# Kernel tuning notes

Hardware: AMD Instinct MI355X
Metric: run time of the kernel (lower is better)

The kernel has to match this reference:

```python
import jax, jax.numpy as jnp
import numpy as np

N = 50000          # nodes
E = 625000         # edges
H = 128            # hidden_dim
L = 4              # num_layers
G = 2000           # number of graphs in batch
NODE_F = 9
EDGE_F = 4
LN_EPS = 1e-5


def setup_inputs() -> dict:
    key = jax.random.key(0)
    ks = jax.random.split(key, 14)
    s = 0.05
    return {
        "x": jax.random.normal(ks[0], (N, NODE_F), jnp.float32),
        "edge_index": jax.random.randint(ks[1], (2, E), 0, N, dtype=jnp.int32),
        "edge_attr": jax.random.normal(ks[2], (E, EDGE_F), jnp.float32),
        "batch": jnp.sort(jax.random.randint(ks[3], (N,), 0, G, dtype=jnp.int32)),
        # node / edge encoders
        "Wn": jax.random.normal(ks[4], (NODE_F, H), jnp.float32) * s,
        "bn": jnp.zeros((H,), jnp.float32),
        "We": jax.random.normal(ks[5], (EDGE_F, H), jnp.float32) * s,
        "be": jnp.zeros((H,), jnp.float32),
        # per-layer GINE MLP params (stacked over layers)
        "W1": jax.random.normal(ks[6], (L, H, 2 * H), jnp.float32) * s,
        "b1": jnp.zeros((L, 2 * H), jnp.float32),
        "W2": jax.random.normal(ks[7], (L, 2 * H, H), jnp.float32) * s,
        "b2": jnp.zeros((L, H), jnp.float32),
        # per-layer LayerNorm params
        "gamma": jnp.ones((L, H), jnp.float32),
        "beta": jnp.zeros((L, H), jnp.float32),
    }


def reference(x, edge_index, edge_attr, batch, Wn, bn, We, be, W1, b1, W2, b2, gamma, beta):
    h = x @ Wn + bn                       # [N, H]
    ea = edge_attr @ We + be              # [E, H]
    src, dst = edge_index[0], edge_index[1]
    for l in range(L):
        res = h
        # GINEConv (eps=0): out = mlp(x + sum_j relu(x_j + e_ij))
        msg = jax.nn.relu(h[src] + ea)                              # [E, H] gather+add+relu
        agg = jax.ops.segment_sum(msg, dst, num_segments=N)        # scatter-sum -> [N, H]
        z = h + agg
        z = jax.nn.relu(z @ W1[l] + b1[l]) @ W2[l] + b2[l]          # 2-layer MLP
        mu = jnp.mean(z, axis=-1, keepdims=True)
        var = jnp.mean((z - mu) ** 2, axis=-1, keepdims=True)
        z = (z - mu) * jax.lax.rsqrt(var + LN_EPS) * gamma[l] + beta[l]
        h = jax.nn.relu(z) + res                                    # relu + residual
    # global_add_pool
    return jax.ops.segment_sum(h, batch, num_segments=G)            # [G, H]
```

## Files before the change

### kernel.cpp

```cpp
#include <hip/hip_runtime.h>

typedef unsigned short ushort_t;
typedef __attribute__((ext_vector_type(8))) __bf16 bf16x8;
typedef __attribute__((ext_vector_type(4))) float f32x4;

#define HD 128
#define NL 4
#define SCAN_C 2048

__device__ __forceinline__ ushort_t f2bf(float f){
  unsigned u = __builtin_bit_cast(unsigned, f);
  unsigned r = (u + 0x7FFFu + ((u >> 16) & 1u)) >> 16;
  return (ushort_t)r;
}

__device__ __forceinline__ float bf2f(ushort_t u){
  unsigned v = ((unsigned)u) << 16;
  return __builtin_bit_cast(float, v);
}

__device__ __forceinline__ f32x4 mfma16(bf16x8 a, bf16x8 b, f32x4 c){
  return __builtin_amdgcn_mfma_f32_16x16x32_bf16(a, b, c, 0, 0, 0);
}

__global__ void hist_kernel(const int* __restrict__ dst, int* __restrict__ deg, int E){
  int e = blockIdx.x * 256 + threadIdx.x;
  if (e < E) atomicAdd(&deg[dst[e]], 1);
}

__global__ void ghist_kernel(const int* __restrict__ batch, int* __restrict__ gdeg, int N){
  int n = blockIdx.x * 256 + threadIdx.x;
  if (n < N) atomicAdd(&gdeg[batch[n]], 1);
}

__global__ void scan_part(const int* __restrict__ in, int* __restrict__ bsum, int n){
  int b = blockIdx.x, tid = threadIdx.x;
  int base = b * SCAN_C + tid * 8;
  int s = 0;
  if (base + 8 <= n){
    int4 a = *(const int4*)(in + base);
    int4 c = *(const int4*)(in + base + 4);
    s = a.x + a.y + a.z + a.w + c.x + c.y + c.z + c.w;
  } else {
    #pragma unroll
    for (int k = 0; k < 8; ++k) if (base + k < n) s += in[base + k];
  }
  #pragma unroll
  for (int o = 1; o < 64; o <<= 1) s += __shfl_xor(s, o, 64);
  __shared__ int ws[4];
  int lane = tid & 63, wid = tid >> 6;
  if (lane == 0) ws[wid] = s;
  __syncthreads();
  if (tid == 0) bsum[b] = ws[0] + ws[1] + ws[2] + ws[3];
}

__global__ void scan_top(const int* __restrict__ bsum, int* __restrict__ bofs,
                         int* __restrict__ outn, int B){
  int tid = threadIdx.x;
  int v = (tid < B) ? bsum[tid] : 0;
  int lane = tid & 63, wid = tid >> 6;
  int inc = v;
  #pragma unroll
  for (int o = 1; o < 64; o <<= 1){
    int t = __shfl_up(inc, o, 64);
    if (lane >= o) inc += t;
  }
  __shared__ int ws[4];
  if (lane == 63) ws[wid] = inc;
  __syncthreads();
  int wprev = 0;
  for (int i = 0; i < wid; ++i) wprev += ws[i];
  if (tid < B) bofs[tid] = inc - v + wprev;
  if (tid == 0) *outn = ws[0] + ws[1] + ws[2] + ws[3];
}

__global__ void scan_final(const int* __restrict__ in, const int* __restrict__ bofs,
                           int* __restrict__ out, int* __restrict__ cur, int n){
  int b = blockIdx.x, tid = threadIdx.x;
  int base = b * SCAN_C + tid * 8;
  int v[8];
  if (base + 8 <= n){
    *(int4*)(v)     = *(const int4*)(in + base);
    *(int4*)(v + 4) = *(const int4*)(in + base + 4);
  } else {
    #pragma unroll
    for (int k = 0; k < 8; ++k) v[k] = (base + k < n) ? in[base + k] : 0;
  }
  int tsum = 0;
  #pragma unroll
  for (int k = 0; k < 8; ++k) tsum += v[k];
  int lane = tid & 63, wid = tid >> 6;
  int inc = tsum;
  #pragma unroll
  for (int o = 1; o < 64; o <<= 1){
    int t = __shfl_up(inc, o, 64);
    if (lane >= o) inc += t;
  }
  __shared__ int ws[4];
  if (lane == 63) ws[wid] = inc;
  __syncthreads();
  int run = bofs[b] + inc - tsum;
  for (int i = 0; i < wid; ++i) run += ws[i];
  #pragma unroll
  for (int k = 0; k < 8; ++k){
    int i = base + k;
    if (i < n){
      out[i] = run;
      if (cur) cur[i] = run;
      run += v[k];
    }
  }
}

__global__ void scatter_kernel(const int* __restrict__ dst, int* __restrict__ cursor,
                               int* __restrict__ perm, int E){
  int e = blockIdx.x * 256 + threadIdx.x;
  if (e < E){
    int d = dst[e];
    int p = atomicAdd(&cursor[d], 1);
    perm[p] = e;
  }
}

__global__ void permute_kernel(const int* __restrict__ perm, const int* __restrict__ src,
                               const float4* __restrict__ ea, int* __restrict__ srcs_s,
                               float4* __restrict__ ea4p, int E){
  int p = blockIdx.x * 256 + threadIdx.x;
  if (p < E){
    int e = perm[p];
    srcs_s[p] = src[e];
    ea4p[p] = ea[e];
  }
}

__global__ void wconv_kernel(const float* __restrict__ W1, const float* __restrict__ W2,
                             ushort_t* __restrict__ W1t, ushort_t* __restrict__ W2t){
  int i = blockIdx.x * 256 + threadIdx.x;
  if (i < NL * 32768){
    int l = i >> 15, r = i & 32767;
    int n = r >> 7, k = r & 127;
    W1t[i] = f2bf(W1[l * 32768 + k * 256 + n]);
  } else {
    int i2 = i - NL * 32768;
    int l = i2 >> 15, r = i2 & 32767;
    int n = r >> 8, k = r & 255;
    W2t[i2] = f2bf(W2[l * 32768 + k * 128 + n]);
  }
}

__global__ void encoder_kernel(const float* __restrict__ x, const float* __restrict__ Wn,
                               const float* __restrict__ bn, float* __restrict__ h,
                               ushort_t* __restrict__ hb, int N){
  int n = blockIdx.x, j = threadIdx.x;
  float acc = bn[j];
  #pragma unroll
  for (int k = 0; k < 9; ++k) acc = fmaf(x[n * 9 + k], Wn[k * HD + j], acc);
  h[(size_t)n * HD + j] = acc;
  hb[(size_t)n * HD + j] = f2bf(acc);
}

__global__ void agg_kernel(const float* __restrict__ h, const ushort_t* __restrict__ hb,
                           const int* __restrict__ off, const int* __restrict__ srcs,
                           const float4* __restrict__ ea4, const float* __restrict__ We,
                           const float* __restrict__ be, ushort_t* __restrict__ z, int N){
  int n = blockIdx.x, j = threadIdx.x;
  float w0 = We[j], w1 = We[HD + j], w2 = We[2 * HD + j], w3 = We[3 * HD + j];
  float bj = be[j];
  int s = off[n], e = off[n + 1];
  float acc = h[(size_t)n * HD + j];
  int i = s;
  for (; i + 8 <= e; i += 8){
    int s0 = srcs[i],     s1 = srcs[i + 1], s2 = srcs[i + 2], s3 = srcs[i + 3];
    int s4 = srcs[i + 4], s5 = srcs[i + 5], s6 = srcs[i + 6], s7 = srcs[i + 7];
    ushort_t g0 = hb[(size_t)s0 * HD + j];
    ushort_t g1 = hb[(size_t)s1 * HD + j];
    ushort_t g2 = hb[(size_t)s2 * HD + j];
    ushort_t g3 = hb[(size_t)s3 * HD + j];
    ushort_t g4 = hb[(size_t)s4 * HD + j];
    ushort_t g5 = hb[(size_t)s5 * HD + j];
    ushort_t g6 = hb[(size_t)s6 * HD + j];
    ushort_t g7 = hb[(size_t)s7 * HD + j];
    {
      float4 a0 = ea4[i], a1 = ea4[i + 1], a2 = ea4[i + 2], a3 = ea4[i + 3];
      float e0 = fmaf(a0.x, w0, fmaf(a0.y, w1, fmaf(a0.z, w2, fmaf(a0.w, w3, bj))));
      float e1 = fmaf(a1.x, w0, fmaf(a1.y, w1, fmaf(a1.z, w2, fmaf(a1.w, w3, bj))));
      float e2 = fmaf(a2.x, w0, fmaf(a2.y, w1, fmaf(a2.z, w2, fmaf(a2.w, w3, bj))));
      float e3 = fmaf(a3.x, w0, fmaf(a3.y, w1, fmaf(a3.z, w2, fmaf(a3.w, w3, bj))));
      acc += fmaxf(bf2f(g0) + e0, 0.f);
      acc += fmaxf(bf2f(g1) + e1, 0.f);
      acc += fmaxf(bf2f(g2) + e2, 0.f);
      acc += fmaxf(bf2f(g3) + e3, 0.f);
    }
    {
      float4 a4 = ea4[i + 4], a5 = ea4[i + 5], a6 = ea4[i + 6], a7 = ea4[i + 7];
      float e4 = fmaf(a4.x, w0, fmaf(a4.y, w1, fmaf(a4.z, w2, fmaf(a4.w, w3, bj))));
      float e5 = fmaf(a5.x, w0, fmaf(a5.y, w1, fmaf(a5.z, w2, fmaf(a5.w, w3, bj))));
      float e6 = fmaf(a6.x, w0, fmaf(a6.y, w1, fmaf(a6.z, w2, fmaf(a6.w, w3, bj))));
      float e7 = fmaf(a7.x, w0, fmaf(a7.y, w1, fmaf(a7.z, w2, fmaf(a7.w, w3, bj))));
      acc += fmaxf(bf2f(g4) + e4, 0.f);
      acc += fmaxf(bf2f(g5) + e5, 0.f);
      acc += fmaxf(bf2f(g6) + e6, 0.f);
      acc += fmaxf(bf2f(g7) + e7, 0.f);
    }
  }
  for (; i + 4 <= e; i += 4){
    int s0 = srcs[i], s1 = srcs[i + 1], s2 = srcs[i + 2], s3 = srcs[i + 3];
    float4 a0 = ea4[i], a1 = ea4[i + 1], a2 = ea4[i + 2], a3 = ea4[i + 3];
    float h0 = bf2f(hb[(size_t)s0 * HD + j]);
    float h1 = bf2f(hb[(size_t)s1 * HD + j]);
    float h2 = bf2f(hb[(size_t)s2 * HD + j]);
    float h3 = bf2f(hb[(size_t)s3 * HD + j]);
    float e0 = fmaf(a0.x, w0, fmaf(a0.y, w1, fmaf(a0.z, w2, fmaf(a0.w, w3, bj))));
    float e1 = fmaf(a1.x, w0, fmaf(a1.y, w1, fmaf(a1.z, w2, fmaf(a1.w, w3, bj))));
    float e2 = fmaf(a2.x, w0, fmaf(a2.y, w1, fmaf(a2.z, w2, fmaf(a2.w, w3, bj))));
    float e3 = fmaf(a3.x, w0, fmaf(a3.y, w1, fmaf(a3.z, w2, fmaf(a3.w, w3, bj))));
    acc += fmaxf(h0 + e0, 0.f);
    acc += fmaxf(h1 + e1, 0.f);
    acc += fmaxf(h2 + e2, 0.f);
    acc += fmaxf(h3 + e3, 0.f);
  }
  for (; i < e; ++i){
    int sc = srcs[i];
    float4 a = ea4[i];
    float eav = fmaf(a.x, w0, fmaf(a.y, w1, fmaf(a.z, w2, fmaf(a.w, w3, bj))));
    acc += fmaxf(bf2f(hb[(size_t)sc * HD + j]) + eav, 0.f);
  }
  z[(size_t)n * HD + j] = f2bf(acc);
}

__global__ __launch_bounds__(512, 4) void mlp_fused_kernel(
    const ushort_t* __restrict__ zin, const ushort_t* __restrict__ W1t,
    const float* __restrict__ b1, const ushort_t* __restrict__ W2t,
    const float* __restrict__ b2, const float* __restrict__ gamma,
    const float* __restrict__ beta, float* __restrict__ h,
    ushort_t* __restrict__ hb, int N){
  extern __shared__ char lds[];
  int tid = threadIdx.x;
  int r0 = blockIdx.x * 128;
  #pragma unroll
  for (int i = 0; i < 4; ++i){
    int g = i * 512 + tid;
    int row = g >> 4, kg = g & 15;
    int lb = row * 256 + ((kg * 16) ^ ((row & 7) << 4));
    int ar = min(r0 + row, N - 1);
    *(bf16x8*)(lds + lb) = *(const bf16x8*)(zin + (size_t)ar * 128 + kg * 8);
  }
  int w = tid >> 6, l = tid & 63;
  int lr = l & 15, lk = l >> 4;
  int wk = w >> 1, wn = w & 1;
  bf16x8 aN[4];
  #pragma unroll
  for (int fm = 0; fm < 4; ++fm)
    aN[fm] = *(const bf16x8*)((const char*)W1t +
              (size_t)(wk * 64 + fm * 16 + lr) * 256 + lk * 16);
  __syncthreads();
  {
    f32x4 acc1[4][4] = {};
    #pragma unroll
    for (int ks = 0; ks < 4; ++ks){
      int kb = ks * 64 + lk * 16;
      bf16x8 aC[4];
      #pragma unroll
      for (int fm = 0; fm < 4; ++fm) aC[fm] = aN[fm];
      if (ks < 3){
        int kbn = (ks + 1) * 64 + lk * 16;
        #pragma unroll
        for (int fm = 0; fm < 4; ++fm)
          aN[fm] = *(const bf16x8*)((const char*)W1t +
                    (size_t)(wk * 64 + fm * 16 + lr) * 256 + kbn);
      }
      bf16x8 b[4];
      #pragma unroll
      for (int fn = 0; fn < 4; ++fn){
        int node = wn * 64 + fn * 16 + lr;
        b[fn] = *(const bf16x8*)(lds + node * 256 + (kb ^ ((node & 7) << 4)));
      }
      #pragma unroll
      for (int fm = 0; fm < 4; ++fm)
        #pragma unroll
        for (int fn = 0; fn < 4; ++fn)
          acc1[fm][fn] = mfma16(aC[fm], b[fn], acc1[fm][fn]);
    }
    __syncthreads();
    #pragma unroll
    for (int fm = 0; fm < 4; ++fm){
      f32x4 bv = *(const f32x4*)(b1 + wk * 64 + fm * 16 + lk * 4);
      int k2b = (wk * 64 + fm * 16 + lk * 4) * 2;
      #pragma unroll
      for (int fn = 0; fn < 4; ++fn){
        int node = wn * 64 + fn * 16 + lr;
        ushort4 tv;
        tv.x = f2bf(fmaxf(acc1[fm][fn][0] + bv[0], 0.f));
        tv.y = f2bf(fmaxf(acc1[fm][fn][1] + bv[1], 0.f));
        tv.z = f2bf(fmaxf(acc1[fm][fn][2] + bv[2], 0.f));
        tv.w = f2bf(fmaxf(acc1[fm][fn][3] + bv[3], 0.f));
        *(ushort4*)(lds + node * 512 + (k2b ^ ((node & 7) << 4))) = tv;
      }
    }
  }
  int wd = w >> 1, wn2 = w & 1;
  bf16x8 a2N[2];
  #pragma unroll
  for (int fm = 0; fm < 2; ++fm)
    a2N[fm] = *(const bf16x8*)((const char*)W2t +
               (size_t)(wd * 32 + fm * 16 + lr) * 512 + lk * 16);
  __syncthreads();
  f32x4 acc2[2][4] = {};
  #pragma unroll
  for (int ks = 0; ks < 8; ++ks){
    int kb = ks * 64 + lk * 16;
    bf16x8 a2C[2];
    #pragma unroll
    for (int fm = 0; fm < 2; ++fm) a2C[fm] = a2N[fm];
    if (ks < 7){
      int kbn = (ks + 1) * 64 + lk * 16;
      #pragma unroll
      for (int fm = 0; fm < 2; ++fm)
        a2N[fm] = *(const bf16x8*)((const char*)W2t +
                   (size_t)(wd * 32 + fm * 16 + lr) * 512 + kbn);
    }
    bf16x8 bt2[4];
    #pragma unroll
    for (int fn = 0; fn < 4; ++fn){
      int node = wn2 * 64 + fn * 16 + lr;
      bt2[fn] = *(const bf16x8*)(lds + node * 512 + (kb ^ ((node & 7) << 4)));
    }
    #pragma unroll
    for (int fm = 0; fm < 2; ++fm)
      #pragma unroll
      for (int fn = 0; fn < 4; ++fn)
        acc2[fm][fn] = mfma16(a2C[fm], bt2[fn], acc2[fm][fn]);
  }
  __syncthreads();
  float* stat_s = (float*)lds;
  float* stat_q = (float*)(lds + 2048);
  f32x4 b2v[2], gv[2], btv[2];
  #pragma unroll
  for (int fm = 0; fm < 2; ++fm){
    int db = wd * 32 + fm * 16 + lk * 4;
    b2v[fm] = *(const f32x4*)(b2 + db);
    gv[fm]  = *(const f32x4*)(gamma + db);
    btv[fm] = *(const f32x4*)(beta + db);
  }
  #pragma unroll
  for (int fn = 0; fn < 4; ++fn){
    float ss = 0.f, qq = 0.f;
    #pragma unroll
    for (int fm = 0; fm < 2; ++fm)
      #pragma unroll
      for (int r = 0; r < 4; ++r){
        float v = acc2[fm][fn][r] + b2v[fm][r];
        acc2[fm][fn][r] = v;
        ss += v; qq += v * v;
      }
    ss += __shfl_xor(ss, 16, 64); ss += __shfl_xor(ss, 32, 64);
    qq += __shfl_xor(qq, 16, 64); qq += __shfl_xor(qq, 32, 64);
    if (l < 16){
      int node = wn2 * 64 + fn * 16 + lr;
      stat_s[node * 4 + wd] = ss;
      stat_q[node * 4 + wd] = qq;
    }
  }
  __syncthreads();
  #pragma unroll
  for (int fn = 0; fn < 4; ++fn){
    int node = wn2 * 64 + fn * 16 + lr;
    int gn = r0 + node;
    float ss = stat_s[node * 4 + 0] + stat_s[node * 4 + 1] +
               stat_s[node * 4 + 2] + stat_s[node * 4 + 3];
    float qq = stat_q[node * 4 + 0] + stat_q[node * 4 + 1] +
               stat_q[node * 4 + 2] + stat_q[node * 4 + 3];
    float mean = ss * (1.f / 128.f);
    float rs = rsqrtf(qq * (1.f / 128.f) - mean * mean + 1e-5f);
    if (gn < N){
      #pragma unroll
      for (int fm = 0; fm < 2; ++fm){
        int db = wd * 32 + fm * 16 + lk * 4;
        f32x4 hold = *(const f32x4*)(h + (size_t)gn * HD + db);
        f32x4 ov;
        #pragma unroll
        for (int r = 0; r < 4; ++r)
          ov[r] = fmaxf((acc2[fm][fn][r] - mean) * rs * gv[fm][r] + btv[fm][r], 0.f) + hold[r];
        *(f32x4*)(h + (size_t)gn * HD + db) = ov;
        ushort4 hv;
        hv.x = f2bf(ov[0]); hv.y = f2bf(ov[1]); hv.z = f2bf(ov[2]); hv.w = f2bf(ov[3]);
        *(ushort4*)(hb + (size_t)gn * HD + db) = hv;
      }
    }
  }
}

__global__ void pool_kernel(const float* __restrict__ h, const int* __restrict__ goff,
                            float* __restrict__ outp, int G){
  int g = blockIdx.x, j = threadIdx.x;
  int s = goff[g], e = goff[g + 1];
  float acc = 0.f;
  for (int i = s; i < e; ++i) acc += h[(size_t)i * HD + j];
  outp[(size_t)g * HD + j] = acc;
}

extern "C" void kernel_launch(void* const* d_in, const int* in_sizes, int n_in,
                              void* d_out, int out_size, void* d_ws, size_t ws_size,
                              hipStream_t stream){
  const float* x     = (const float*)d_in[0];
  const int*   ei    = (const int*)  d_in[1];
  const float* eattr = (const float*)d_in[2];
  const int*   batch = (const int*)  d_in[3];
  const float* Wn    = (const float*)d_in[4];
  const float* bn    = (const float*)d_in[5];
  const float* We    = (const float*)d_in[6];
  const float* be    = (const float*)d_in[7];
  const float* W1    = (const float*)d_in[8];
  const float* b1    = (const float*)d_in[9];
  const float* W2    = (const float*)d_in[10];
  const float* b2    = (const float*)d_in[11];
  const float* gamma = (const float*)d_in[12];
  const float* beta  = (const float*)d_in[13];
  float* outp = (float*)d_out;

  int N = in_sizes[3];
  int E = in_sizes[2] / 4;
  int G = out_size / HD;

  char* base = (char*)d_ws;
  size_t o = 0;
  auto alloc = [&](size_t bytes)->char*{
    char* r = base + o; o = (o + bytes + 255) & ~(size_t)255; return r;
  };
  float*    h    = (float*)   alloc((size_t)N * HD * 4);
  ushort_t* hb   = (ushort_t*)alloc((size_t)N * HD * 2);
  ushort_t* z    = (ushort_t*)alloc((size_t)N * HD * 2);
  ushort_t* W1t  = (ushort_t*)alloc((size_t)NL * 2 * HD * HD * 2);
  ushort_t* W2t  = (ushort_t*)alloc((size_t)NL * 2 * HD * HD * 2);
  int* deg    = (int*)alloc((size_t)N * 4);
  int* gdeg   = (int*)alloc((size_t)G * 4);
  int* off    = (int*)alloc((size_t)(N + 1) * 4);
  int* goff   = (int*)alloc((size_t)(G + 1) * 4);
  int* cursor = (int*)alloc((size_t)N * 4);
  int* bsumN  = (int*)alloc(512 * 4);
  int* bofsN  = (int*)alloc(512 * 4);
  int* bsumG  = (int*)alloc(512 * 4);
  int* bofsG  = (int*)alloc(512 * 4);
  int* perm   = (int*)alloc((size_t)E * 4);
  int* srcs_s = (int*)alloc((size_t)E * 4);
  float4* ea4p= (float4*)alloc((size_t)E * 16);
  (void)ws_size; (void)n_in;

  const int* src = ei;
  const int* dst = ei + E;

  hipMemsetAsync(deg, 0, (size_t)N * 4, stream);
  hipMemsetAsync(gdeg, 0, (size_t)G * 4, stream);

  hist_kernel<<<(E + 255) / 256, 256, 0, stream>>>(dst, deg, E);
  ghist_kernel<<<(N + 255) / 256, 256, 0, stream>>>(batch, gdeg, N);

  int BN = (N + SCAN_C - 1) / SCAN_C;
  int BG = (G + SCAN_C - 1) / SCAN_C;
  scan_part<<<BN, 256, 0, stream>>>(deg, bsumN, N);
  scan_top<<<1, 256, 0, stream>>>(bsumN, bofsN, off + N, BN);
  scan_final<<<BN, 256, 0, stream>>>(deg, bofsN, off, cursor, N);
  scan_part<<<BG, 256, 0, stream>>>(gdeg, bsumG, G);
  scan_top<<<1, 256, 0, stream>>>(bsumG, bofsG, goff + G, BG);
  scan_final<<<BG, 256, 0, stream>>>(gdeg, bofsG, goff, (int*)nullptr, G);

  scatter_kernel<<<(E + 255) / 256, 256, 0, stream>>>(dst, cursor, perm, E);
  permute_kernel<<<(E + 255) / 256, 256, 0, stream>>>(perm, src, (const float4*)eattr,
                                                      srcs_s, ea4p, E);
  wconv_kernel<<<(2 * NL * 32768) / 256, 256, 0, stream>>>(W1, W2, W1t, W2t);
  encoder_kernel<<<N, HD, 0, stream>>>(x, Wn, bn, h, hb, N);

  int mblocks = (N + 127) / 128;
  for (int l = 0; l < NL; ++l){
    agg_kernel<<<N, HD, 0, stream>>>(h, hb, off, srcs_s, ea4p, We, be, z, N);
    mlp_fused_kernel<<<mblocks, 512, 65536, stream>>>(
        z, W1t + (size_t)l * 2 * HD * HD, b1 + l * 2 * HD,
        W2t + (size_t)l * 2 * HD * HD, b2 + l * HD,
        gamma + l * HD, beta + l * HD, h, hb, N);
  }
  pool_kernel<<<G, HD, 0, stream>>>(h, goff, outp, G);
}
```

Before: 421.8 us.

## Use wave-per-node aggregation with paired bf16 loads, derive graph offsets from sorted batch

The aggregation kernel now assigns one 64-lane wave per node instead of a 128-thread block, with each lane handling two adjacent feature channels through 32-bit loads. This halves the number of gather instructions, makes per-edge index and edge-attr loads shared across fewer threads, and packs four nodes per block. The self term now reads the bf16 copy of h instead of the fp32 one, which adds rounding error. Graph offsets for pooling are computed directly from boundaries in the sorted batch array, replacing the histogram plus three scan kernels.

```diff
diff --git a/kernel.cpp b/kernel.cpp
--- a/kernel.cpp
+++ b/kernel.cpp
@@ -28,9 +28,15 @@
   if (e < E) atomicAdd(&deg[dst[e]], 1);
 }
 
-__global__ void ghist_kernel(const int* __restrict__ batch, int* __restrict__ gdeg, int N){
+__global__ void gbound_kernel(const int* __restrict__ batch, int* __restrict__ goff,
+                              int N, int G){
   int n = blockIdx.x * 256 + threadIdx.x;
-  if (n < N) atomicAdd(&gdeg[batch[n]], 1);
+  if (n >= N) return;
+  int bc = batch[n];
+  int bp = (n == 0) ? -1 : batch[n - 1];
+  for (int g = bp + 1; g <= bc; ++g) goff[g] = n;
+  if (n == N - 1)
+    for (int g = bc + 1; g <= G; ++g) goff[g] = N;
 }
 
 __global__ void scan_part(const int* __restrict__ in, int* __restrict__ bsum, int n){
@@ -159,73 +165,57 @@
   hb[(size_t)n * HD + j] = f2bf(acc);
 }
 
-__global__ void agg_kernel(const float* __restrict__ h, const ushort_t* __restrict__ hb,
-                           const int* __restrict__ off, const int* __restrict__ srcs,
-                           const float4* __restrict__ ea4, const float* __restrict__ We,
-                           const float* __restrict__ be, ushort_t* __restrict__ z, int N){
-  int n = blockIdx.x, j = threadIdx.x;
-  float w0 = We[j], w1 = We[HD + j], w2 = We[2 * HD + j], w3 = We[3 * HD + j];
-  float bj = be[j];
-  int s = off[n], e = off[n + 1];
-  float acc = h[(size_t)n * HD + j];
+__global__ __launch_bounds__(256) void agg_kernel(
+    const ushort_t* __restrict__ hb, const int* __restrict__ off,
+    const int* __restrict__ srcs, const float4* __restrict__ ea4,
+    const float* __restrict__ We, const float* __restrict__ be,
+    ushort_t* __restrict__ z, int N){
+  int node = blockIdx.x * 4 + (threadIdx.x >> 6);
+  if (node >= N) return;
+  int l = threadIdx.x & 63;
+  int j0 = l * 2;
+  float w00 = We[j0],          w01 = We[j0 + 1];
+  float w10 = We[HD + j0],     w11 = We[HD + j0 + 1];
+  float w20 = We[2 * HD + j0], w21 = We[2 * HD + j0 + 1];
+  float w30 = We[3 * HD + j0], w31 = We[3 * HD + j0 + 1];
+  float be0 = be[j0], be1 = be[j0 + 1];
+  int s = off[node], e = off[node + 1];
+  unsigned hs = *(const unsigned*)(hb + (size_t)node * HD + j0);
+  float acc0 = bf2f((ushort_t)(hs & 0xFFFFu));
+  float acc1 = bf2f((ushort_t)(hs >> 16));
   int i = s;
   for (; i + 8 <= e; i += 8){
     int s0 = srcs[i],     s1 = srcs[i + 1], s2 = srcs[i + 2], s3 = srcs[i + 3];
     int s4 = srcs[i + 4], s5 = srcs[i + 5], s6 = srcs[i + 6], s7 = srcs[i + 7];
-    ushort_t g0 = hb[(size_t)s0 * HD + j];
-    ushort_t g1 = hb[(size_t)s1 * HD + j];
-    ushort_t g2 = hb[(size_t)s2 * HD + j];
-    ushort_t g3 = hb[(size_t)s3 * HD + j];
-    ushort_t g4 = hb[(size_t)s4 * HD + j];
-    ushort_t g5 = hb[(size_t)s5 * HD + j];
-    ushort_t g6 = hb[(size_t)s6 * HD + j];
-    ushort_t g7 = hb[(size_t)s7 * HD + j];
-    {
-      float4 a0 = ea4[i], a1 = ea4[i + 1], a2 = ea4[i + 2], a3 = ea4[i + 3];
-      float e0 = fmaf(a0.x, w0, fmaf(a0.y, w1, fmaf(a0.z, w2, fmaf(a0.w, w3, bj))));
-      float e1 = fmaf(a1.x, w0, fmaf(a1.y, w1, fmaf(a1.z, w2, fmaf(a1.w, w3, bj))));
-      float e2 = fmaf(a2.x, w0, fmaf(a2.y, w1, fmaf(a2.z, w2, fmaf(a2.w, w3, bj))));
-      float e3 = fmaf(a3.x, w0, fmaf(a3.y, w1, fmaf(a3.z, w2, fmaf(a3.w, w3, bj))));
-      acc += fmaxf(bf2f(g0) + e0, 0.f);
-      acc += fmaxf(bf2f(g1) + e1, 0.f);
-      acc += fmaxf(bf2f(g2) + e2, 0.f);
-      acc += fmaxf(bf2f(g3) + e3, 0.f);
-    }
-    {
-      float4 a4 = ea4[i + 4], a5 = ea4[i + 5], a6 = ea4[i + 6], a7 = ea4[i + 7];
-      float e4 = fmaf(a4.x, w0, fmaf(a4.y, w1, fmaf(a4.z, w2, fmaf(a4.w, w3, bj))));
-      float e5 = fmaf(a5.x, w0, fmaf(a5.y, w1, fmaf(a5.z, w2, fmaf(a5.w, w3, bj))));
-      float e6 = fmaf(a6.x, w0, fmaf(a6.y, w1, fmaf(a6.z, w2, fmaf(a6.w, w3, bj))));
-      float e7 = fmaf(a7.x, w0, fmaf(a7.y, w1, fmaf(a7.z, w2, fmaf(a7.w, w3, bj))));
-      acc += fmaxf(bf2f(g4) + e4, 0.f);
-      acc += fmaxf(bf2f(g5) + e5, 0.f);
-      acc += fmaxf(bf2f(g6) + e6, 0.f);
-      acc += fmaxf(bf2f(g7) + e7, 0.f);
-    }
-  }
-  for (; i + 4 <= e; i += 4){
-    int s0 = srcs[i], s1 = srcs[i + 1], s2 = srcs[i + 2], s3 = srcs[i + 3];
-    float4 a0 = ea4[i], a1 = ea4[i + 1], a2 = ea4[i + 2], a3 = ea4[i + 3];
-    float h0 = bf2f(hb[(size_t)s0 * HD + j]);
-    float h1 = bf2f(hb[(size_t)s1 * HD + j]);
-    float h2 = bf2f(hb[(size_t)s2 * HD + j]);
-    float h3 = bf2f(hb[(size_t)s3 * HD + j]);
-    float e0 = fmaf(a0.x, w0, fmaf(a0.y, w1, fmaf(a0.z, w2, fmaf(a0.w, w3, bj))));
-    float e1 = fmaf(a1.x, w0, fmaf(a1.y, w1, fmaf(a1.z, w2, fmaf(a1.w, w3, bj))));
-    float e2 = fmaf(a2.x, w0, fmaf(a2.y, w1, fmaf(a2.z, w2, fmaf(a2.w, w3, bj))));
-    float e3 = fmaf(a3.x, w0, fmaf(a3.y, w1, fmaf(a3.z, w2, fmaf(a3.w, w3, bj))));
-    acc += fmaxf(h0 + e0, 0.f);
-    acc += fmaxf(h1 + e1, 0.f);
-    acc += fmaxf(h2 + e2, 0.f);
-    acc += fmaxf(h3 + e3, 0.f);
+    unsigned g0 = *(const unsigned*)(hb + (size_t)s0 * HD + j0);
+    unsigned g1 = *(const unsigned*)(hb + (size_t)s1 * HD + j0);
+    unsigned g2 = *(const unsigned*)(hb + (size_t)s2 * HD + j0);
+    unsigned g3 = *(const unsigned*)(hb + (size_t)s3 * HD + j0);
+    unsigned g4 = *(const unsigned*)(hb + (size_t)s4 * HD + j0);
+    unsigned g5 = *(const unsigned*)(hb + (size_t)s5 * HD + j0);
+    unsigned g6 = *(const unsigned*)(hb + (size_t)s6 * HD + j0);
+    unsigned g7 = *(const unsigned*)(hb + (size_t)s7 * HD + j0);
+    unsigned gs[8] = {g0, g1, g2, g3, g4, g5, g6, g7};
+    #pragma unroll
+    for (int k = 0; k < 8; ++k){
+      float4 a = ea4[i + k];
+      float e0 = fmaf(a.x, w00, fmaf(a.y, w10, fmaf(a.z, w20, fmaf(a.w, w30, be0))));
+      float e1 = fmaf(a.x, w01, fmaf(a.y, w11, fmaf(a.z, w21, fmaf(a.w, w31, be1))));
+      acc0 += fmaxf(bf2f((ushort_t)(gs[k] & 0xFFFFu)) + e0, 0.f);
+      acc1 += fmaxf(bf2f((ushort_t)(gs[k] >> 16)) + e1, 0.f);
+    }
   }
   for (; i < e; ++i){
     int sc = srcs[i];
+    unsigned g = *(const unsigned*)(hb + (size_t)sc * HD + j0);
     float4 a = ea4[i];
-    float eav = fmaf(a.x, w0, fmaf(a.y, w1, fmaf(a.z, w2, fmaf(a.w, w3, bj))));
-    acc += fmaxf(bf2f(hb[(size_t)sc * HD + j]) + eav, 0.f);
-  }
-  z[(size_t)n * HD + j] = f2bf(acc);
+    float e0 = fmaf(a.x, w00, fmaf(a.y, w10, fmaf(a.z, w20, fmaf(a.w, w30, be0))));
+    float e1 = fmaf(a.x, w01, fmaf(a.y, w11, fmaf(a.z, w21, fmaf(a.w, w31, be1))));
+    acc0 += fmaxf(bf2f((ushort_t)(g & 0xFFFFu)) + e0, 0.f);
+    acc1 += fmaxf(bf2f((ushort_t)(g >> 16)) + e1, 0.f);
+  }
+  unsigned outw = (unsigned)f2bf(acc0) | ((unsigned)f2bf(acc1) << 16);
+  *(unsigned*)(z + (size_t)node * HD + j0) = outw;
 }
 
 __global__ __launch_bounds__(512, 4) void mlp_fused_kernel(
@@ -433,14 +423,11 @@
   ushort_t* W1t  = (ushort_t*)alloc((size_t)NL * 2 * HD * HD * 2);
   ushort_t* W2t  = (ushort_t*)alloc((size_t)NL * 2 * HD * HD * 2);
   int* deg    = (int*)alloc((size_t)N * 4);
-  int* gdeg   = (int*)alloc((size_t)G * 4);
   int* off    = (int*)alloc((size_t)(N + 1) * 4);
   int* goff   = (int*)alloc((size_t)(G + 1) * 4);
   int* cursor = (int*)alloc((size_t)N * 4);
   int* bsumN  = (int*)alloc(512 * 4);
   int* bofsN  = (int*)alloc(512 * 4);
-  int* bsumG  = (int*)alloc(512 * 4);
-  int* bofsG  = (int*)alloc(512 * 4);
   int* perm   = (int*)alloc((size_t)E * 4);
   int* srcs_s = (int*)alloc((size_t)E * 4);
   float4* ea4p= (float4*)alloc((size_t)E * 16);
@@ -450,19 +437,14 @@
   const int* dst = ei + E;
 
   hipMemsetAsync(deg, 0, (size_t)N * 4, stream);
-  hipMemsetAsync(gdeg, 0, (size_t)G * 4, stream);
 
   hist_kernel<<<(E + 255) / 256, 256, 0, stream>>>(dst, deg, E);
-  ghist_kernel<<<(N + 255) / 256, 256, 0, stream>>>(batch, gdeg, N);
+  gbound_kernel<<<(N + 255) / 256, 256, 0, stream>>>(batch, goff, N, G);
 
   int BN = (N + SCAN_C - 1) / SCAN_C;
-  int BG = (G + SCAN_C - 1) / SCAN_C;
   scan_part<<<BN, 256, 0, stream>>>(deg, bsumN, N);
   scan_top<<<1, 256, 0, stream>>>(bsumN, bofsN, off + N, BN);
   scan_final<<<BN, 256, 0, stream>>>(deg, bofsN, off, cursor, N);
-  scan_part<<<BG, 256, 0, stream>>>(gdeg, bsumG, G);
-  scan_top<<<1, 256, 0, stream>>>(bsumG, bofsG, goff + G, BG);
-  scan_final<<<BG, 256, 0, stream>>>(gdeg, bofsG, goff, (int*)nullptr, G);
 
   scatter_kernel<<<(E + 255) / 256, 256, 0, stream>>>(dst, cursor, perm, E);
   permute_kernel<<<(E + 255) / 256, 256, 0, stream>>>(perm, src, (const float4*)eattr,
@@ -470,9 +452,10 @@
   wconv_kernel<<<(2 * NL * 32768) / 256, 256, 0, stream>>>(W1, W2, W1t, W2t);
   encoder_kernel<<<N, HD, 0, stream>>>(x, Wn, bn, h, hb, N);
 
+  int ablocks = (N + 3) / 4;
   int mblocks = (N + 127) / 128;
   for (int l = 0; l < NL; ++l){
-    agg_kernel<<<N, HD, 0, stream>>>(h, hb, off, srcs_s, ea4p, We, be, z, N);
+    agg_kernel<<<ablocks, 256, 0, stream>>>(hb, off, srcs_s, ea4p, We, be, z, N);
     mlp_fused_kernel<<<mblocks, 512, 65536, stream>>>(
         z, W1t + (size_t)l * 2 * HD * HD, b1 + l * 2 * HD,
         W2t + (size_t)l * 2 * HD * HD, b2 + l * HD,
```

Result: slower. 442.6 us (+4.9%).
